# Kernel tuning notes

Hardware: AMD Instinct MI355X
Metric: run time of the kernel (lower is better)

## Reference

```python
import jax, jax.numpy as jnp
import numpy as np

B, T, F, UNITS = 256, 256, 64, 512


def _lstm(x, W, Uw, b):
    """Keras-style LSTM with activation=relu, recurrent_activation=sigmoid.
    x: [B,T,F_in]; W: [F_in,4U]; Uw: [U,4U]; b: [4U]. Gate order i,f,c,o.
    Returns (all_h [B,T,U], last_h [B,U])."""
    n = Uw.shape[0]
    xg = jnp.einsum('btf,fg->btg', x, W) + b  # precompute input projections [B,T,4U]

    def step(carry, xg_t):
        h, c = carry
        z = xg_t + h @ Uw  # [B,4U]
        i, f, g, o = jnp.split(z, 4, axis=-1)
        i = jax.nn.sigmoid(i)
        f = jax.nn.sigmoid(f)
        g = jax.nn.relu(g)          # candidate activation = relu
        o = jax.nn.sigmoid(o)
        c = f * c + i * g
        h = o * jax.nn.relu(c)      # output activation = relu
        return (h, c), h

    h0 = jnp.zeros((x.shape[0], n), x.dtype)
    (hT, _), hs = jax.lax.scan(step, (h0, jnp.zeros_like(h0)), jnp.swapaxes(xg, 0, 1))
    return jnp.swapaxes(hs, 0, 1), hT


def setup_inputs() -> dict:
    key = jax.random.key(0)
    ks = jax.random.split(key, 8)
    s = 0.05
    return {
        'x':  jax.random.normal(ks[0], (B, T, F), jnp.float32),
        'W1': jax.random.normal(ks[1], (F, 4 * UNITS), jnp.float32) * s,
        'U1': jax.random.normal(ks[2], (UNITS, 4 * UNITS), jnp.float32) * s,
        'b1': jnp.zeros((4 * UNITS,), jnp.float32),
        'W2': jax.random.normal(ks[3], (UNITS, 4 * UNITS), jnp.float32) * s,
        'U2': jax.random.normal(ks[4], (UNITS, 4 * UNITS), jnp.float32) * s,
        'b2': jnp.zeros((4 * UNITS,), jnp.float32),
        'Wd': jax.random.normal(ks[5], (UNITS, 1), jnp.float32) * s,
        'bd': jnp.zeros((1,), jnp.float32),
    }


def reference(x, W1, U1, b1, W2, U2, b2, Wd, bd):
    h1, _ = _lstm(x, W1, U1, b1)      # return_sequences=True; dropout identity at inference
    _, h2 = _lstm(h1, W2, U2, b2)     # return_sequences=False -> last hidden state
    return jax.nn.sigmoid(h2 @ Wd + bd)  # [B,1]
```

## Files before the change

### kernel.cpp

```cpp
#include <hip/hip_runtime.h>
#include <hip/hip_bf16.h>

#define B_  256
#define T_  256
#define F_  64
#define U_  512
#define NG_ 2048
#define BU_ (B_ * U_)

typedef __attribute__((ext_vector_type(8))) short short8;
typedef __attribute__((ext_vector_type(16))) float floatx16;

__device__ __forceinline__ unsigned short f2bf(float f) {
    union { float f; unsigned int u; } v; v.f = f;
    unsigned int u = v.u;
    return (unsigned short)((u + 0x7FFFu + ((u >> 16) & 1u)) >> 16);
}
__device__ __forceinline__ float bf2f(unsigned short s) {
    union { unsigned int u; float f; } v; v.u = ((unsigned int)s) << 16;
    return v.f;
}

__global__ void cast_x_kernel(const float* __restrict__ x,
                              unsigned short* __restrict__ xb, int n) {
    int i = blockIdx.x * blockDim.x + threadIdx.x;
    if (i < n) xb[i] = f2bf(x[i]);
}

__global__ void pack32_kernel(const float* __restrict__ W, const float* __restrict__ Uw,
                              unsigned short* __restrict__ dst, int KT, int KX) {
    long tid = (long)blockIdx.x * blockDim.x + threadIdx.x;
    long total = 16L * 4 * KT * 512;
    if (tid >= total) return;
    int j    = (int)(tid & 7);
    int lane = (int)((tid >> 3) & 63);
    int p512 = (int)(tid >> 9);
    int kt   = p512 % KT;
    int q    = (p512 / KT) & 3;
    int ug   = p512 / (KT * 4);
    int srcn = q * U_ + ug * 32 + (lane & 31);
    int k    = kt * 16 + (lane >> 5) * 8 + j;
    float v  = (k < KX) ? W[(long)k * NG_ + srcn] : Uw[(long)(k - KX) * NG_ + srcn];
    dst[tid] = f2bf(v);
}

__device__ __forceinline__ short8 llc_load(const unsigned short* p) {
    short8 r;
    asm volatile("global_load_dwordx4 %0, %1, off sc0 sc1" : "=v"(r) : "v"(p));
    return r;
}
__device__ __forceinline__ void sys_store_u32(unsigned int* p, unsigned int v) {
    asm volatile("global_store_dword %0, %1, off sc0 sc1" :: "v"(p), "v"(v) : "memory");
}
#define VMWAIT(N) asm volatile("s_waitcnt vmcnt(" #N ")" ::: "memory")
__device__ __forceinline__ void dep8(short8& x) { asm volatile("" : "+v"(x)); }

#define MFMA32(a, b, c) __builtin_amdgcn_mfma_f32_32x32x16_bf16(a, b, c, 0, 0, 0)

__device__ __forceinline__ void lds_barrier() {
    __builtin_amdgcn_sched_barrier(0);
    asm volatile("s_waitcnt lgkmcnt(0)" ::: "memory");
    __builtin_amdgcn_s_barrier();
    __builtin_amdgcn_sched_barrier(0);
}

template<int N, int M>
__device__ __forceinline__ void wait_fresh(short8 (&d)[M], const unsigned short* b, int koff) {
    int g = 0;
    for (;;) {
        VMWAIT(0);
        __builtin_amdgcn_sched_barrier(0);
        #pragma unroll
        for (int i = 0; i < N; ++i) dep8(d[i]);
        bool bad = false;
        #pragma unroll
        for (int i = 0; i < N; ++i) {
            union { short8 s; unsigned int w[4]; } u; u.s = d[i];
            #pragma unroll
            for (int j = 0; j < 4; ++j) bad |= (u.w[j] == 0xFFFFFFFFu);
        }
        if (__ballot(bad) == 0ull) break;
        if (++g > (1 << 15)) break;
        #pragma unroll
        for (int i = 0; i < N; ++i) d[i] = llc_load(b + i * 16 + koff);
    }
}

__global__ __launch_bounds__(512, 1) void lstm_persist(
    const unsigned short* __restrict__ xb,
    const unsigned short* __restrict__ P1,
    const unsigned short* __restrict__ P2,
    const float* __restrict__ b1, const float* __restrict__ b2,
    unsigned short* __restrict__ h1h, unsigned short* __restrict__ h2h)
{
    const int bid  = blockIdx.x;
    const bool isL1 = (bid < 128);
    const int sub  = isL1 ? bid : (bid - 128);
    const int mo   = sub & 7;
    const int ug   = sub >> 3;
    const int tid  = threadIdx.x;
    const int w    = tid >> 6;
    const int lane = tid & 63;
    const int arow = lane & 31;
    const int koff = (lane >> 5) * 8;
    const int row  = mo * 32 + arow;

    __shared__ float red[8][4][32][33];
    __shared__ float cst[32][32];
    __shared__ float bias_s[4][32];

    for (int i = tid; i < 1024; i += 512) cst[i >> 5][i & 31] = 0.f;
    if (tid < 128) {
        const float* bb = isL1 ? b1 : b2;
        bias_s[tid >> 5][tid & 31] = bb[(tid >> 5) * U_ + ug * 32 + (tid & 31)];
    }

    if (isL1) {
        const int kbase = (w < 4) ? w * 5 : 20 + (w - 4) * 4;
        const int kcnt  = (w < 4) ? 5 : 4;
        short8 wf[4][5];
        {
            const unsigned short* base = P1 + (size_t)ug * (4 * 36 * 512);
            #pragma unroll
            for (int q = 0; q < 4; ++q) {
                #pragma unroll
                for (int i = 0; i < 5; ++i) {
                    if (i < kcnt)
                        wf[q][i] = *(const short8*)(base
                            + ((size_t)(q * 36 + kbase + i) * 64 + lane) * 8);
                }
            }
        }
        __syncthreads();

        for (int k = 0; k < T_; ++k) {
            floatx16 acc[4];
            #pragma unroll
            for (int q = 0; q < 4; ++q) {
                #pragma unroll
                for (int i = 0; i < 16; ++i) acc[q][i] = 0.f;
            }

            if (w == 0) {
                const unsigned short* xbase = xb + ((size_t)row * T_ + k) * F_;
                #pragma unroll
                for (int g = 0; g < 4; ++g) {
                    short8 a = *(const short8*)(xbase + g * 16 + koff);
                    #pragma unroll
                    for (int q = 0; q < 4; ++q) acc[q] = MFMA32(a, wf[q][g], acc[q]);
                }
            }

            if (k >= 1) {
                if (w == 0) {
                    const unsigned short* hb = h1h + (size_t)(k - 1) * BU_
                                               + (size_t)row * U_;
                    short8 fa[1];
                    fa[0] = llc_load(hb + koff);
                    wait_fresh<1>(fa, hb, koff);
                    dep8(fa[0]);
                    #pragma unroll
                    for (int q = 0; q < 4; ++q) acc[q] = MFMA32(fa[0], wf[q][4], acc[q]);
                } else if (w < 4) {
                    const unsigned short* hb = h1h + (size_t)(k - 1) * BU_
                                               + (size_t)row * U_ + (kbase - 4) * 16;
                    short8 fa[5];
                    #pragma unroll
                    for (int i = 0; i < 5; ++i) fa[i] = llc_load(hb + i * 16 + koff);
                    wait_fresh<5>(fa, hb, koff);
                    #pragma unroll
                    for (int i = 0; i < 5; ++i) {
                        dep8(fa[i]);
                        #pragma unroll
                        for (int q = 0; q < 4; ++q) acc[q] = MFMA32(fa[i], wf[q][i], acc[q]);
                    }
                } else {
                    const unsigned short* hb = h1h + (size_t)(k - 1) * BU_
                                               + (size_t)row * U_ + (kbase - 4) * 16;
                    short8 fa[4];
                    #pragma unroll
                    for (int i = 0; i < 4; ++i) fa[i] = llc_load(hb + i * 16 + koff);
                    wait_fresh<4>(fa, hb, koff);
                    #pragma unroll
                    for (int i = 0; i < 4; ++i) {
                        dep8(fa[i]);
                        #pragma unroll
                        for (int q = 0; q < 4; ++q) acc[q] = MFMA32(fa[i], wf[q][i], acc[q]);
                    }
                }
            }

            #pragma unroll
            for (int r = 0; r < 16; ++r) {
                int rr = (r & 3) + 8 * (r >> 2) + 4 * (lane >> 5);
                #pragma unroll
                for (int q = 0; q < 4; ++q) red[w][q][rr][arow] = acc[q][r];
            }
            lds_barrier();

            {
                int r = tid >> 4, u2 = (tid & 15) * 2;
                unsigned int pk = 0;
                #pragma unroll
                for (int du = 0; du < 2; ++du) {
                    int u = u2 + du;
                    float zi = 0.f, zf = 0.f, zg = 0.f, zo = 0.f;
                    #pragma unroll
                    for (int ww = 0; ww < 8; ++ww) {
                        zi += red[ww][0][r][u];
                        zf += red[ww][1][r][u];
                        zg += red[ww][2][r][u];
                        zo += red[ww][3][r][u];
                    }
                    zi += bias_s[0][u]; zf += bias_s[1][u];
                    zg += bias_s[2][u]; zo += bias_s[3][u];
                    float si = 1.f / (1.f + __expf(-zi));
                    float sf = 1.f / (1.f + __expf(-zf));
                    float so = 1.f / (1.f + __expf(-zo));
                    float gg = zg > 0.f ? zg : 0.f;
                    float cn = sf * cst[r][u] + si * gg;
                    cst[r][u] = cn;
                    float hn = so * (cn > 0.f ? cn : 0.f);
                    pk |= ((unsigned int)f2bf(hn)) << (16 * du);
                }
                unsigned int* hp = (unsigned int*)(h1h + (size_t)k * BU_
                                   + (size_t)(mo * 32 + r) * U_ + ug * 32 + u2);
                sys_store_u32(hp, pk);
            }
            lds_barrier();
        }
    } else {
        short8 wf[4][8];
        {
            const unsigned short* base = P2 + (size_t)ug * (4 * 64 * 512);
            #pragma unroll
            for (int q = 0; q < 4; ++q) {
                #pragma unroll
                for (int i = 0; i < 8; ++i)
                    wf[q][i] = *(const short8*)(base
                        + ((size_t)(q * 64 + w * 8 + i) * 64 + lane) * 8);
            }
        }
        __syncthreads();

        for (int t = 0; t < T_; ++t) {
            floatx16 acc[4];
            #pragma unroll
            for (int q = 0; q < 4; ++q) {
                #pragma unroll
                for (int i = 0; i < 16; ++i) acc[q][i] = 0.f;
            }

            const bool isU2 = (w >= 4);
            if (!isU2 || t >= 1) {
                const unsigned short* hb = isU2
                    ? h2h + (size_t)(t - 1) * BU_ + (size_t)row * U_ + (w - 4) * 128
                    : h1h + (size_t)t * BU_       + (size_t)row * U_ + w * 128;
                short8 fb[8];
                #pragma unroll
                for (int i = 0; i < 8; ++i) fb[i] = llc_load(hb + i * 16 + koff);
                wait_fresh<8>(fb, hb, koff);
                #pragma unroll
                for (int i = 0; i < 8; ++i) {
                    dep8(fb[i]);
                    #pragma unroll
                    for (int q = 0; q < 4; ++q) acc[q] = MFMA32(fb[i], wf[q][i], acc[q]);
                }
            }

            #pragma unroll
            for (int r = 0; r < 16; ++r) {
                int rr = (r & 3) + 8 * (r >> 2) + 4 * (lane >> 5);
                #pragma unroll
                for (int q = 0; q < 4; ++q) red[w][q][rr][arow] = acc[q][r];
            }
            lds_barrier();

            {
                int r = tid >> 4, u2 = (tid & 15) * 2;
                unsigned int pk = 0;
                #pragma unroll
                for (int du = 0; du < 2; ++du) {
                    int u = u2 + du;
                    float zi = 0.f, zf = 0.f, zg = 0.f, zo = 0.f;
                    #pragma unroll
                    for (int ww = 0; ww < 8; ++ww) {
                        zi += red[ww][0][r][u];
                        zf += red[ww][1][r][u];
                        zg += red[ww][2][r][u];
                        zo += red[ww][3][r][u];
                    }
                    zi += bias_s[0][u]; zf += bias_s[1][u];
                    zg += bias_s[2][u]; zo += bias_s[3][u];
                    float si = 1.f / (1.f + __expf(-zi));
                    float sf = 1.f / (1.f + __expf(-zf));
                    float so = 1.f / (1.f + __expf(-zo));
                    float gg = zg > 0.f ? zg : 0.f;
                    float cn = sf * cst[r][u] + si * gg;
                    cst[r][u] = cn;
                    float hn = so * (cn > 0.f ? cn : 0.f);
                    pk |= ((unsigned int)f2bf(hn)) << (16 * du);
                }
                unsigned int* hp = (unsigned int*)(h2h + (size_t)t * BU_
                                   + (size_t)(mo * 32 + r) * U_ + ug * 32 + u2);
                sys_store_u32(hp, pk);
            }
            lds_barrier();
        }
    }
}

__global__ void dense_kernel(const unsigned short* __restrict__ h2,
                             const float* __restrict__ Wd,
                             const float* __restrict__ bd,
                             float* __restrict__ out) {
    int b = blockIdx.x;
    int lane = threadIdx.x;
    const unsigned short* hp = h2 + (long)b * U_ + lane * 8;
    float sum = 0.f;
    #pragma unroll
    for (int j = 0; j < 8; ++j) sum += bf2f(hp[j]) * Wd[lane * 8 + j];
    #pragma unroll
    for (int off = 32; off; off >>= 1) sum += __shfl_down(sum, off);
    if (lane == 0) out[b] = 1.f / (1.f + __expf(-(sum + bd[0])));
}

extern "C" void kernel_launch(void* const* d_in, const int* in_sizes, int n_in,
                              void* d_out, int out_size, void* d_ws, size_t ws_size,
                              hipStream_t stream) {
    const float* x  = (const float*)d_in[0];
    const float* W1 = (const float*)d_in[1];
    const float* U1 = (const float*)d_in[2];
    const float* b1 = (const float*)d_in[3];
    const float* W2 = (const float*)d_in[4];
    const float* U2 = (const float*)d_in[5];
    const float* b2 = (const float*)d_in[6];
    const float* Wd = (const float*)d_in[7];
    const float* bd = (const float*)d_in[8];
    float* out = (float*)d_out;

    char* ws = (char*)d_ws;
    size_t off = 0;
    unsigned short* xb  = (unsigned short*)(ws + off); off += (size_t)B_ * T_ * F_ * 2;
    unsigned short* P1  = (unsigned short*)(ws + off); off += (size_t)16 * 4 * 36 * 512 * 2;
    unsigned short* P2  = (unsigned short*)(ws + off); off += (size_t)16 * 4 * 64 * 512 * 2;
    unsigned short* h1h = (unsigned short*)(ws + off); off += (size_t)T_ * BU_ * 2;
    unsigned short* h2h = (unsigned short*)(ws + off); off += (size_t)T_ * BU_ * 2;

    (void)hipMemsetAsync(h1h, 0xFF, (size_t)2 * T_ * BU_ * 2, stream);

    int n = B_ * T_ * F_;
    cast_x_kernel<<<(n + 255) / 256, 256, 0, stream>>>(x, xb, n);
    {
        long tot1 = 16L * 4 * 36 * 512;
        pack32_kernel<<<(int)((tot1 + 255) / 256), 256, 0, stream>>>(W1, U1, P1, 36, 64);
        long tot2 = 16L * 4 * 64 * 512;
        pack32_kernel<<<(int)((tot2 + 255) / 256), 256, 0, stream>>>(W2, U2, P2, 64, 512);
    }

    lstm_persist<<<256, 512, 0, stream>>>(xb, P1, P2, b1, b2, h1h, h2h);

    dense_kernel<<<B_, 64, 0, stream>>>(h2h + (size_t)(T_ - 1) * BU_,
                                        Wd, bd, out);
}
```

Measured before the change: 1.187 ms.

## Spin on a single probe load before fetching recurrent state; keep cell state in registers

Adds a wait routine that polls one 16-byte chunk of the previous step's hidden state until it stops holding the 0xFFFFFFFF sentinel, then issues the remaining loads and runs the full freshness check. It is used for the recurrent reads in both layers. The aim is to cut redundant multi-chunk reloads while spinning on cross-block data. The layer-1 wave 0 now issues its recurrent load before the input-projection MFMAs so the two overlap. Cell state and bias move from LDS into registers, and the reduction reads float2 values from a padded layout, which removes LDS traffic in the gate epilogue. The probe assumes the first chunk lands no earlier than the others, and the full check is kept as a fallback.

```diff
diff --git a/kernel.cpp b/kernel.cpp
--- a/kernel.cpp
+++ b/kernel.cpp
@@ -84,6 +84,25 @@
         #pragma unroll
         for (int i = 0; i < N; ++i) d[i] = llc_load(b + i * 16 + koff);
     }
+}
+
+template<int N, int M>
+__device__ __forceinline__ void wait_fresh_probe(short8 (&d)[M], const unsigned short* b, int koff) {
+    int g = 0;
+    for (;;) {
+        VMWAIT(0);
+        __builtin_amdgcn_sched_barrier(0);
+        dep8(d[0]);
+        union { short8 s; unsigned int w[4]; } u; u.s = d[0];
+        bool bad = (u.w[0] == 0xFFFFFFFFu) | (u.w[1] == 0xFFFFFFFFu)
+                 | (u.w[2] == 0xFFFFFFFFu) | (u.w[3] == 0xFFFFFFFFu);
+        if (__ballot(bad) == 0ull) break;
+        if (++g > (1 << 15)) break;
+        d[0] = llc_load(b + koff);
+    }
+    #pragma unroll
+    for (int i = 1; i < N; ++i) d[i] = llc_load(b + i * 16 + koff);
+    wait_fresh<N>(d, b, koff);
 }
 
 __global__ __launch_bounds__(512, 1) void lstm_persist(
@@ -105,14 +124,19 @@
     const int koff = (lane >> 5) * 8;
     const int row  = mo * 32 + arow;
 
-    __shared__ float red[8][4][32][33];
-    __shared__ float cst[32][32];
-    __shared__ float bias_s[4][32];
-
-    for (int i = tid; i < 1024; i += 512) cst[i >> 5][i & 31] = 0.f;
-    if (tid < 128) {
+    __shared__ float red[8][4][32][34];
+
+    const int er = tid >> 4;
+    const int eu = (tid & 15) * 2;
+    float cs0 = 0.f, cs1 = 0.f;
+    float bg[4][2];
+    {
         const float* bb = isL1 ? b1 : b2;
-        bias_s[tid >> 5][tid & 31] = bb[(tid >> 5) * U_ + ug * 32 + (tid & 31)];
+        #pragma unroll
+        for (int q = 0; q < 4; ++q) {
+            bg[q][0] = bb[q * U_ + ug * 32 + eu];
+            bg[q][1] = bb[q * U_ + ug * 32 + eu + 1];
+        }
     }
 
     if (isL1) {
@@ -142,6 +166,10 @@
             }
 
             if (w == 0) {
+                const unsigned short* hb = h1h + (size_t)(k - 1) * BU_
+                                           + (size_t)row * U_;
+                short8 fa[1];
+                if (k >= 1) fa[0] = llc_load(hb + koff);
                 const unsigned short* xbase = xb + ((size_t)row * T_ + k) * F_;
                 #pragma unroll
                 for (int g = 0; g < 4; ++g) {
@@ -149,25 +177,20 @@
                     #pragma unroll
                     for (int q = 0; q < 4; ++q) acc[q] = MFMA32(a, wf[q][g], acc[q]);
                 }
-            }
-
-            if (k >= 1) {
-                if (w == 0) {
-                    const unsigned short* hb = h1h + (size_t)(k - 1) * BU_
-                                               + (size_t)row * U_;
-                    short8 fa[1];
-                    fa[0] = llc_load(hb + koff);
-                    wait_fresh<1>(fa, hb, koff);
+                if (k >= 1) {
+                    wait_fresh_probe<1>(fa, hb, koff);
                     dep8(fa[0]);
                     #pragma unroll
                     for (int q = 0; q < 4; ++q) acc[q] = MFMA32(fa[0], wf[q][4], acc[q]);
-                } else if (w < 4) {
+                }
+            } else if (k >= 1) {
+                if (w < 4) {
                     const unsigned short* hb = h1h + (size_t)(k - 1) * BU_
                                                + (size_t)row * U_ + (kbase - 4) * 16;
                     short8 fa[5];
                     #pragma unroll
                     for (int i = 0; i < 5; ++i) fa[i] = llc_load(hb + i * 16 + koff);
-                    wait_fresh<5>(fa, hb, koff);
+                    wait_fresh_probe<5>(fa, hb, koff);
                     #pragma unroll
                     for (int i = 0; i < 5; ++i) {
                         dep8(fa[i]);
@@ -180,7 +203,7 @@
                     short8 fa[4];
                     #pragma unroll
                     for (int i = 0; i < 4; ++i) fa[i] = llc_load(hb + i * 16 + koff);
-                    wait_fresh<4>(fa, hb, koff);
+                    wait_fresh_probe<4>(fa, hb, koff);
                     #pragma unroll
                     for (int i = 0; i < 4; ++i) {
                         dep8(fa[i]);
@@ -199,32 +222,33 @@
             lds_barrier();
 
             {
-                int r = tid >> 4, u2 = (tid & 15) * 2;
-                unsigned int pk = 0;
-                #pragma unroll
-                for (int du = 0; du < 2; ++du) {
-                    int u = u2 + du;
-                    float zi = 0.f, zf = 0.f, zg = 0.f, zo = 0.f;
-                    #pragma unroll
-                    for (int ww = 0; ww < 8; ++ww) {
-                        zi += red[ww][0][r][u];
-                        zf += red[ww][1][r][u];
-                        zg += red[ww][2][r][u];
-                        zo += red[ww][3][r][u];
+                float z[4][2];
+                #pragma unroll
+                for (int q = 0; q < 4; ++q) { z[q][0] = bg[q][0]; z[q][1] = bg[q][1]; }
+                #pragma unroll
+                for (int ww = 0; ww < 8; ++ww) {
+                    #pragma unroll
+                    for (int q = 0; q < 4; ++q) {
+                        float2 v = *reinterpret_cast<const float2*>(&red[ww][q][er][eu]);
+                        z[q][0] += v.x; z[q][1] += v.y;
                     }
-                    zi += bias_s[0][u]; zf += bias_s[1][u];
-                    zg += bias_s[2][u]; zo += bias_s[3][u];
-                    float si = 1.f / (1.f + __expf(-zi));
-                    float sf = 1.f / (1.f + __expf(-zf));
-                    float so = 1.f / (1.f + __expf(-zo));
-                    float gg = zg > 0.f ? zg : 0.f;
-                    float cn = sf * cst[r][u] + si * gg;
-                    cst[r][u] = cn;
-                    float hn = so * (cn > 0.f ? cn : 0.f);
-                    pk |= ((unsigned int)f2bf(hn)) << (16 * du);
-                }
+                }
+                float si0 = 1.f / (1.f + __expf(-z[0][0]));
+                float sf0 = 1.f / (1.f + __expf(-z[1][0]));
+                float gg0 = z[2][0] > 0.f ? z[2][0] : 0.f;
+                float so0 = 1.f / (1.f + __expf(-z[3][0]));
+                cs0 = sf0 * cs0 + si0 * gg0;
+                float hn0 = so0 * (cs0 > 0.f ? cs0 : 0.f);
+                float si1 = 1.f / (1.f + __expf(-z[0][1]));
+                float sf1 = 1.f / (1.f + __expf(-z[1][1]));
+                float gg1 = z[2][1] > 0.f ? z[2][1] : 0.f;
+                float so1 = 1.f / (1.f + __expf(-z[3][1]));
+                cs1 = sf1 * cs1 + si1 * gg1;
+                float hn1 = so1 * (cs1 > 0.f ? cs1 : 0.f);
+                unsigned int pk = (unsigned int)f2bf(hn0)
+                                | ((unsigned int)f2bf(hn1) << 16);
                 unsigned int* hp = (unsigned int*)(h1h + (size_t)k * BU_
-                                   + (size_t)(mo * 32 + r) * U_ + ug * 32 + u2);
+                                   + (size_t)(mo * 32 + er) * U_ + ug * 32 + eu);
                 sys_store_u32(hp, pk);
             }
             lds_barrier();
@@ -259,7 +283,8 @@
                 short8 fb[8];
                 #pragma unroll
                 for (int i = 0; i < 8; ++i) fb[i] = llc_load(hb + i * 16 + koff);
-                wait_fresh<8>(fb, hb, koff);
+                if (isU2) wait_fresh_probe<8>(fb, hb, koff);
+                else      wait_fresh<8>(fb, hb, koff);
                 #pragma unroll
                 for (int i = 0; i < 8; ++i) {
                     dep8(fb[i]);
@@ -277,32 +302,33 @@
             lds_barrier();
 
             {
-                int r = tid >> 4, u2 = (tid & 15) * 2;
-                unsigned int pk = 0;
-                #pragma unroll
-                for (int du = 0; du < 2; ++du) {
-                    int u = u2 + du;
-                    float zi = 0.f, zf = 0.f, zg = 0.f, zo = 0.f;
-                    #pragma unroll
-                    for (int ww = 0; ww < 8; ++ww) {
-                        zi += red[ww][0][r][u];
-                        zf += red[ww][1][r][u];
-                        zg += red[ww][2][r][u];
-                        zo += red[ww][3][r][u];
+                float z[4][2];
+                #pragma unroll
+                for (int q = 0; q < 4; ++q) { z[q][0] = bg[q][0]; z[q][1] = bg[q][1]; }
+                #pragma unroll
+                for (int ww = 0; ww < 8; ++ww) {
+                    #pragma unroll
+                    for (int q = 0; q < 4; ++q) {
+                        float2 v = *reinterpret_cast<const float2*>(&red[ww][q][er][eu]);
+                        z[q][0] += v.x; z[q][1] += v.y;
                     }
-                    zi += bias_s[0][u]; zf += bias_s[1][u];
-                    zg += bias_s[2][u]; zo += bias_s[3][u];
-                    float si = 1.f / (1.f + __expf(-zi));
-                    float sf = 1.f / (1.f + __expf(-zf));
-                    float so = 1.f / (1.f + __expf(-zo));
-                    float gg = zg > 0.f ? zg : 0.f;
-                    float cn = sf * cst[r][u] + si * gg;
-                    cst[r][u] = cn;
-                    float hn = so * (cn > 0.f ? cn : 0.f);
-                    pk |= ((unsigned int)f2bf(hn)) << (16 * du);
-                }
+                }
+                float si0 = 1.f / (1.f + __expf(-z[0][0]));
+                float sf0 = 1.f / (1.f + __expf(-z[1][0]));
+                float gg0 = z[2][0] > 0.f ? z[2][0] : 0.f;
+                float so0 = 1.f / (1.f + __expf(-z[3][0]));
+                cs0 = sf0 * cs0 + si0 * gg0;
+                float hn0 = so0 * (cs0 > 0.f ? cs0 : 0.f);
+                float si1 = 1.f / (1.f + __expf(-z[0][1]));
+                float sf1 = 1.f / (1.f + __expf(-z[1][1]));
+                float gg1 = z[2][1] > 0.f ? z[2][1] : 0.f;
+                float so1 = 1.f / (1.f + __expf(-z[3][1]));
+                cs1 = sf1 * cs1 + si1 * gg1;
+                float hn1 = so1 * (cs1 > 0.f ? cs1 : 0.f);
+                unsigned int pk = (unsigned int)f2bf(hn0)
+                                | ((unsigned int)f2bf(hn1) << 16);
                 unsigned int* hp = (unsigned int*)(h2h + (size_t)t * BU_
-                                   + (size_t)(mo * 32 + r) * U_ + ug * 32 + u2);
+                                   + (size_t)(mo * 32 + er) * U_ + ug * 32 + eu);
                 sys_store_u32(hp, pk);
             }
             lds_barrier();
```

After: 1.437 ms. 1.21x slower.
